# Kernel tuning notes

Hardware: AMD Instinct MI355X
Metric: run time of the kernel (lower is better)

The kernel has to match this reference:

```python
import jax, jax.numpy as jnp
import numpy as np
import math

L, V, P, D, H, B, S = 6, 32000, 1024, 768, 12, 8, 1024
HD = D // H
NEG = jnp.float32(-1e9)
EPS = 1e-5


def gelu(x):
    return 0.5 * x * (1 + jnp.tanh(math.sqrt(2 / math.pi) * (x + 0.044715 * x ** 3)))


def layer_norm(x, g, b):
    mu = jnp.mean(x, -1, keepdims=True)
    var = jnp.mean((x - mu) ** 2, -1, keepdims=True)
    return (x - mu) * jax.lax.rsqrt(var + EPS) * g + b


def setup_inputs() -> dict:
    key = jax.random.key(0)
    ks = jax.random.split(key, 16)
    tokens = jax.random.randint(ks[0], (B, S), 0, V)
    tok_emb = 0.02 * jax.random.normal(ks[1], (V, D), jnp.float32)
    tok_emb = tok_emb.at[0].set(0.0)  # padding_idx=0 row zeroed
    pos_emb = 0.01 * jax.random.normal(ks[2], (P + 1, D), jnp.float32)
    pos_emb = pos_emb.at[0].set(0.0)  # pos padding row
    return {
        "tokens": tokens,
        "tok_emb": tok_emb,
        "pos_emb": pos_emb,
        "qkv_w": 0.02 * jax.random.normal(ks[3], (L, 3 * D, D), jnp.float32),
        "qkv_b": jnp.zeros((L, 3 * D), jnp.float32),
        "out_w": 0.02 * jax.random.normal(ks[4], (L, D, D), jnp.float32),
        "out_b": jnp.zeros((L, D), jnp.float32),
        "ln1_g": jnp.ones((L, D), jnp.float32),
        "ln1_b": jnp.zeros((L, D), jnp.float32),
        "ff1_w": 0.02 * jax.random.normal(ks[5], (L, 4 * D, D), jnp.float32),
        "ff1_b": jnp.zeros((L, 4 * D), jnp.float32),
        "ff2_w": 0.02 * jax.random.normal(ks[6], (L, D, 4 * D), jnp.float32),
        "ff2_b": jnp.zeros((L, D), jnp.float32),
        "ln2_g": jnp.ones((L, D), jnp.float32),
        "ln2_b": jnp.zeros((L, D), jnp.float32),
    }


def _forward(tokens, tok_emb, pos_emb, qkv_w, qkv_b, out_w, out_b,
             ln1_g, ln1_b, ff1_w, ff1_b, ff2_w, ff2_b, ln2_g, ln2_b):
    pad = tokens == 0  # [B,S] padding mask
    positions = jnp.where(pad, 0, jnp.cumsum((~pad).astype(jnp.int32), axis=-1))
    x = tok_emb[tokens] + pos_emb[positions]  # [B,S,D]

    causal = jnp.triu(jnp.ones((S, S), bool), 1)  # future mask
    mask = causal[None, None] | pad[:, None, None, :]  # [B,1,S,S]
    all_masked = mask.all(-1)  # [B,1,S] rows fully -inf -> zeroed after softmax

    def block(x, p):
        qw, qb, ow, ob, g1, b1, f1w, f1b, f2w, f2b, g2, b2 = p
        qkv = x @ qw.T + qb
        q, k, v = jnp.split(qkv, 3, axis=-1)
        q = q.reshape(B, S, H, HD).transpose(0, 2, 1, 3)
        k = k.reshape(B, S, H, HD).transpose(0, 2, 1, 3)
        v = v.reshape(B, S, H, HD).transpose(0, 2, 1, 3)
        w = jnp.einsum('bhqd,bhkd->bhqk', q, k) / math.sqrt(HD)
        w = jnp.where(mask, NEG, w)
        w = jax.nn.softmax(w, axis=-1)
        w = jnp.where(all_masked[..., None], 0.0, w)
        a = jnp.einsum('bhqk,bhkd->bhqd', w, v)
        a = a.transpose(0, 2, 1, 3).reshape(B, S, D)
        a = a @ ow.T + ob
        x = layer_norm(x + a, g1, b1)
        h = gelu(x @ f1w.T + f1b) @ f2w.T + f2b
        x = layer_norm(x + h, g2, b2)
        return x, None

    params = (qkv_w, qkv_b, out_w, out_b, ln1_g, ln1_b,
              ff1_w, ff1_b, ff2_w, ff2_b, ln2_g, ln2_b)
    x, _ = jax.lax.scan(block, x, params)
    return x, pad


def reference(tokens, tok_emb, pos_emb, qkv_w, qkv_b, out_w, out_b,
              ln1_g, ln1_b, ff1_w, ff1_b, ff2_w, ff2_b, ln2_g, ln2_b):
    return _forward(tokens, tok_emb, pos_emb, qkv_w, qkv_b, out_w, out_b,
                    ln1_g, ln1_b, ff1_w, ff1_b, ff2_w, ff2_b, ln2_g, ln2_b)
```

## Files before the change

### kernel.cpp

```cpp
#include <hip/hip_runtime.h>
#include <hip/hip_bf16.h>
#include <math.h>

#define LNUM 6
#define DIM  768
#define HID  3072
#define QKVD 2304
#define NH   12
#define HD   64
#define BB   8
#define SS   1024
#define MTOT (BB*SS)

typedef _Float16 f16x8 __attribute__((ext_vector_type(8)));
typedef _Float16 f16x4 __attribute__((ext_vector_type(4)));
typedef float    f32x4 __attribute__((ext_vector_type(4)));

__device__ __forceinline__ void gload_lds16(const void* g, void* l) {
    __builtin_amdgcn_global_load_lds(
        (const __attribute__((address_space(1))) void*)g,
        (__attribute__((address_space(3))) void*)l, 16, 0, 0);
}

__global__ __launch_bounds__(1024) void pos_kernel(const int* __restrict__ tokens,
                                                   int* __restrict__ positions,
                                                   float* __restrict__ pad_out) {
    const int b = blockIdx.x;
    const int s = threadIdx.x;
    const int tok = tokens[b*SS + s];
    const int np = (tok != 0) ? 1 : 0;
    __shared__ int sc[SS];
    sc[s] = np;
    __syncthreads();
    for (int off = 1; off < SS; off <<= 1) {
        int v = sc[s];
        if (s >= off) v += sc[s - off];
        __syncthreads();
        sc[s] = v;
        __syncthreads();
    }
    positions[b*SS + s] = np ? sc[s] : 0;
    pad_out[b*SS + s]   = np ? 0.0f : 1.0f;
}

__global__ __launch_bounds__(256) void embed_kernel(const int* __restrict__ tokens,
                                                    const int* __restrict__ positions,
                                                    const float* __restrict__ tok_emb,
                                                    const float* __restrict__ pos_emb,
                                                    float* __restrict__ x32,
                                                    _Float16* __restrict__ x16) {
    const int gid = blockIdx.x * 256 + threadIdx.x;
    const int m = gid / (DIM/4);
    const int c = (gid % (DIM/4)) * 4;
    const int tok = tokens[m];
    const int p   = positions[m];
    const float4 te = *(const float4*)(tok_emb + (size_t)tok*DIM + c);
    const float4 pe = *(const float4*)(pos_emb + (size_t)p  *DIM + c);
    float4 r;
    r.x = te.x + pe.x; r.y = te.y + pe.y; r.z = te.z + pe.z; r.w = te.w + pe.w;
    *(float4*)(x32 + (size_t)m*DIM + c) = r;
    f16x4 h; h[0] = (_Float16)r.x; h[1] = (_Float16)r.y; h[2] = (_Float16)r.z; h[3] = (_Float16)r.w;
    *(f16x4*)(x16 + (size_t)m*DIM + c) = h;
}

__global__ __launch_bounds__(256) void cvt16_kernel(const float* __restrict__ in,
                                                    _Float16* __restrict__ out, int n4) {
    const int i = blockIdx.x * 256 + threadIdx.x;
    if (i < n4) {
        const float4 v = ((const float4*)in)[i];
        f16x4 h; h[0] = (_Float16)v.x; h[1] = (_Float16)v.y; h[2] = (_Float16)v.z; h[3] = (_Float16)v.w;
        ((f16x4*)out)[i] = h;
    }
}

template<int EPI>
__global__ __launch_bounds__(256) void hgemm_kernel(const _Float16* __restrict__ A,
                                                    const _Float16* __restrict__ W,
                                                    const float* __restrict__ bias,
                                                    const float* __restrict__ res,
                                                    void* __restrict__ Cout,
                                                    int M, int N, int K) {
    __shared__ char lds[32768];
    const int tid  = threadIdx.x;
    const int w    = tid >> 6;
    const int lane = tid & 63;
    const int wr = w >> 1, wc = w & 1;
    const int bm = blockIdx.y, bn = blockIdx.x;
    const _Float16* Arow = A + (size_t)(bm*128)*K;
    const _Float16* Brow = W + (size_t)(bn*128)*K;

    f32x4 acc[4][4] = {};

    for (int k0 = 0; k0 < K; k0 += 64) {
        #pragma unroll
        for (int i = 0; i < 4; i++) {
            const int p  = (i*4 + w)*64 + lane;
            const int r  = p >> 3;
            const int ul = (p & 7) ^ (r & 7);
            gload_lds16(Arow + (size_t)r*K + k0 + ul*8, lds + (i*4 + w)*1024);
            gload_lds16(Brow + (size_t)r*K + k0 + ul*8, lds + 16384 + (i*4 + w)*1024);
        }
        __syncthreads();
        #pragma unroll
        for (int ks = 0; ks < 2; ks++) {
            f16x8 af[4], bf[4];
            #pragma unroll
            for (int mi = 0; mi < 4; mi++) {
                const int ra = wr*64 + mi*16 + (lane & 15);
                const int ua = (ks*4 + (lane >> 4)) ^ (ra & 7);
                af[mi] = *(const f16x8*)(lds + ra*128 + ua*16);
                const int rb = wc*64 + mi*16 + (lane & 15);
                const int ub = (ks*4 + (lane >> 4)) ^ (rb & 7);
                bf[mi] = *(const f16x8*)(lds + 16384 + rb*128 + ub*16);
            }
            #pragma unroll
            for (int mi = 0; mi < 4; mi++)
                #pragma unroll
                for (int ni = 0; ni < 4; ni++)
                    acc[mi][ni] = __builtin_amdgcn_mfma_f32_16x16x32_f16(af[mi], bf[ni], acc[mi][ni], 0, 0, 0);
        }
        __syncthreads();
    }

    const int lr = lane >> 4, lc = lane & 15;
    #pragma unroll
    for (int mi = 0; mi < 4; mi++) {
        #pragma unroll
        for (int r = 0; r < 4; r++) {
            const int row = bm*128 + wr*64 + mi*16 + lr*4 + r;
            #pragma unroll
            for (int ni = 0; ni < 4; ni++) {
                const int col = bn*128 + wc*64 + ni*16 + lc;
                float v = acc[mi][ni][r] + bias[col];
                if (EPI == 1) v += res[(size_t)row*N + col];
                if (EPI == 2) {
                    const float u = v;
                    v = 0.5f*u*(1.0f + tanhf(0.7978845608028654f*(u + 0.044715f*u*u*u)));
                    ((_Float16*)Cout)[(size_t)row*N + col] = (_Float16)v;
                } else {
                    ((float*)Cout)[(size_t)row*N + col] = v;
                }
            }
        }
    }
}

__global__ __launch_bounds__(256) void attn_kernel(const float* __restrict__ qkv,
                                                   const int* __restrict__ tokens,
                                                   _Float16* __restrict__ aout) {
    __shared__ float Ks[64][64];
    __shared__ float Vs[64][64];
    __shared__ int tf[64];
    const int gx = blockIdx.x;
    const int qblk = 3 - (gx / 96);
    const int bh = gx % 96;
    const int h = bh % NH, b = bh / NH;
    const int w = threadIdx.x >> 6, lane = threadIdx.x & 63;
    const int ql = qblk*256 + lane*4 + w;
    const size_t rowq = (size_t)(b*SS + ql);
    const float* kv0 = qkv + (size_t)b*SS*QKVD + DIM + h*HD;

    f32x4 qv[16];
    const float* qp = qkv + rowq*QKVD + h*HD;
    #pragma unroll
    for (int i = 0; i < 16; i++) {
        qv[i] = *(const f32x4*)(qp + i*4);
        qv[i] *= 0.125f;
    }
    f32x4 av[16] = {};
    float m = -1e30f, lsum = 0.0f;

    const int ntile = qblk*4 + 4;
    for (int t = 0; t < ntile; t++) {
        const int k0 = t*64;
        __syncthreads();
        for (int p4 = threadIdx.x; p4 < 1024; p4 += 256) {
            const int r = p4 >> 4, c = (p4 & 15)*4;
            const float* src = kv0 + (size_t)(k0 + r)*QKVD + c;
            *(float4*)&Ks[r][c] = *(const float4*)src;
            *(float4*)&Vs[r][c] = *(const float4*)(src + DIM);
        }
        if (threadIdx.x < 64) tf[threadIdx.x] = tokens[b*SS + k0 + threadIdx.x];
        __syncthreads();
        for (int kk = 0; kk < 64; kk++) {
            if (tf[kk] == 0) continue;
            const int k = k0 + kk;
            f32x4 s4 = {};
            #pragma unroll
            for (int i = 0; i < 16; i++)
                s4 += qv[i] * *(const f32x4*)&Ks[kk][i*4];
            const float s = (s4[0] + s4[1]) + (s4[2] + s4[3]);
            const bool valid = (k <= ql);
            if (valid && s > m + 8.0f) {
                const float f = __expf(m - s);
                lsum *= f;
                #pragma unroll
                for (int i = 0; i < 16; i++) av[i] *= f;
                m = s;
            }
            const float p = valid ? __expf(s - m) : 0.0f;
            lsum += p;
            #pragma unroll
            for (int i = 0; i < 16; i++)
                av[i] += p * *(const f32x4*)&Vs[kk][i*4];
        }
    }
    const float inv = (lsum > 0.0f) ? 1.0f / lsum : 0.0f;
    _Float16* op = aout + rowq*DIM + h*HD;
    #pragma unroll
    for (int i = 0; i < 16; i++) {
        f16x4 o;
        o[0] = (_Float16)(av[i][0]*inv); o[1] = (_Float16)(av[i][1]*inv);
        o[2] = (_Float16)(av[i][2]*inv); o[3] = (_Float16)(av[i][3]*inv);
        *(f16x4*)(op + i*4) = o;
    }
}

__global__ __launch_bounds__(256) void ln_kernel(const float* __restrict__ in,
                                                 const float* __restrict__ g,
                                                 const float* __restrict__ b,
                                                 float* __restrict__ out32,
                                                 _Float16* __restrict__ out16) {
    const int row = blockIdx.x;
    const int t = threadIdx.x;
    const float* xr = in + (size_t)row*DIM;
    const float v0 = xr[t], v1 = xr[t+256], v2 = xr[t+512];
    __shared__ float red[4];
    __shared__ float stat[2];
    const int lane = t & 63, wid = t >> 6;
    float s = v0 + v1 + v2;
    #pragma unroll
    for (int off = 32; off; off >>= 1) s += __shfl_down(s, off);
    if (lane == 0) red[wid] = s;
    __syncthreads();
    if (t == 0) stat[0] = (red[0]+red[1]+red[2]+red[3]) * (1.0f/DIM);
    __syncthreads();
    const float mean = stat[0];
    const float d0 = v0-mean, d1 = v1-mean, d2 = v2-mean;
    float sq = d0*d0 + d1*d1 + d2*d2;
    #pragma unroll
    for (int off = 32; off; off >>= 1) sq += __shfl_down(sq, off);
    __syncthreads();
    if (lane == 0) red[wid] = sq;
    __syncthreads();
    if (t == 0) stat[1] = rsqrtf((red[0]+red[1]+red[2]+red[3]) * (1.0f/DIM) + 1e-5f);
    __syncthreads();
    const float rstd = stat[1];
    float* orow = out32 + (size_t)row*DIM;
    _Float16* hrow = out16 + (size_t)row*DIM;
    const float o0 = d0*rstd*g[t]     + b[t];
    const float o1 = d1*rstd*g[t+256] + b[t+256];
    const float o2 = d2*rstd*g[t+512] + b[t+512];
    orow[t]     = o0; orow[t+256] = o1; orow[t+512] = o2;
    hrow[t]     = (_Float16)o0; hrow[t+256] = (_Float16)o1; hrow[t+512] = (_Float16)o2;
}

extern "C" void kernel_launch(void* const* d_in, const int* in_sizes, int n_in,
                              void* d_out, int out_size, void* d_ws, size_t ws_size,
                              hipStream_t stream) {
    const int*   tokens  = (const int*)  d_in[0];
    const float* tok_emb = (const float*)d_in[1];
    const float* pos_emb = (const float*)d_in[2];
    const float* qkv_w   = (const float*)d_in[3];
    const float* qkv_b   = (const float*)d_in[4];
    const float* out_w   = (const float*)d_in[5];
    const float* out_b   = (const float*)d_in[6];
    const float* ln1_g   = (const float*)d_in[7];
    const float* ln1_b   = (const float*)d_in[8];
    const float* ff1_w   = (const float*)d_in[9];
    const float* ff1_b   = (const float*)d_in[10];
    const float* ff2_w   = (const float*)d_in[11];
    const float* ff2_b   = (const float*)d_in[12];
    const float* ln2_g   = (const float*)d_in[13];
    const float* ln2_b   = (const float*)d_in[14];

    char* ws = (char*)d_ws;
    size_t off = 0;
    auto carve = [&](size_t bytes) { char* p = ws + off; off += (bytes + 255) & ~(size_t)255; return p; };
    int*      positions = (int*)     carve((size_t)MTOT*4);
    float*    x32    = (float*)      carve((size_t)MTOT*DIM*4);
    _Float16* x16    = (_Float16*)   carve((size_t)MTOT*DIM*2);
    float*    ln1o32 = (float*)      carve((size_t)MTOT*DIM*4);
    _Float16* ln1o16 = (_Float16*)   carve((size_t)MTOT*DIM*2);
    float*    y32    = (float*)      carve((size_t)MTOT*DIM*4);
    float*    qkv32  = (float*)      carve((size_t)MTOT*QKVD*4);
    _Float16* a16    = (_Float16*)   carve((size_t)MTOT*DIM*2);
    _Float16* h16    = (_Float16*)   carve((size_t)MTOT*HID*2);
    _Float16* wq16   = (_Float16*)   carve((size_t)QKVD*DIM*2);
    _Float16* wo16   = (_Float16*)   carve((size_t)DIM*DIM*2);
    _Float16* w116   = (_Float16*)   carve((size_t)HID*DIM*2);
    _Float16* w216   = (_Float16*)   carve((size_t)DIM*HID*2);

    float* outx    = (float*)d_out;
    float* pad_out = outx + (size_t)MTOT*DIM;

    pos_kernel<<<BB, SS, 0, stream>>>(tokens, positions, pad_out);
    embed_kernel<<<(MTOT*(DIM/4))/256, 256, 0, stream>>>(tokens, positions, tok_emb, pos_emb, x32, x16);

    for (int l = 0; l < LNUM; l++) {
        cvt16_kernel<<<(QKVD*DIM/4)/256, 256, 0, stream>>>(qkv_w + (size_t)l*QKVD*DIM, wq16, QKVD*DIM/4);
        cvt16_kernel<<<(DIM*DIM/4)/256,  256, 0, stream>>>(out_w + (size_t)l*DIM*DIM,  wo16, DIM*DIM/4);
        cvt16_kernel<<<(HID*DIM/4)/256,  256, 0, stream>>>(ff1_w + (size_t)l*HID*DIM,  w116, HID*DIM/4);
        cvt16_kernel<<<(DIM*HID/4)/256,  256, 0, stream>>>(ff2_w + (size_t)l*DIM*HID,  w216, DIM*HID/4);

        hgemm_kernel<0><<<dim3(QKVD/128, MTOT/128), 256, 0, stream>>>(
            x16, wq16, qkv_b + (size_t)l*QKVD, nullptr, qkv32, MTOT, QKVD, DIM);
        attn_kernel<<<BB*NH*4, 256, 0, stream>>>(qkv32, tokens, a16);
        hgemm_kernel<1><<<dim3(DIM/128, MTOT/128), 256, 0, stream>>>(
            a16, wo16, out_b + (size_t)l*DIM, x32, y32, MTOT, DIM, DIM);
        ln_kernel<<<MTOT, 256, 0, stream>>>(y32, ln1_g + (size_t)l*DIM, ln1_b + (size_t)l*DIM, ln1o32, ln1o16);
        hgemm_kernel<2><<<dim3(HID/128, MTOT/128), 256, 0, stream>>>(
            ln1o16, w116, ff1_b + (size_t)l*HID, nullptr, h16, MTOT, HID, DIM);
        hgemm_kernel<1><<<dim3(DIM/128, MTOT/128), 256, 0, stream>>>(
            h16, w216, ff2_b + (size_t)l*DIM, ln1o32, y32, MTOT, DIM, HID);
        ln_kernel<<<MTOT, 256, 0, stream>>>(
            y32, ln2_g + (size_t)l*DIM, ln2_b + (size_t)l*DIM, (l == LNUM-1) ? outx : x32, x16);
    }
}
```

Before: 5.309 ms.

## Split attention into split-K partial kernel with combine pass and fp16 keys

The QKV GEMM now writes Q and V as separate fp32 buffers and K as fp16. Attention is restructured from one thread per query over 256-query blocks into 64-query tiles whose key range is split across four waves, each keeping its own running softmax state. A second kernel merges the four partials. Keys are read straight from global memory and scored with fp16 dot2 instructions, with no LDS staging or block barriers. This raises parallelism and balances causal work, at the cost of extra partial-result traffic through a scratch buffer aliased with h16, fp16 rounding of Q and K scores, and uncoalesced per-thread row loads.

```diff
diff --git a/kernel.cpp b/kernel.cpp
--- a/kernel.cpp
+++ b/kernel.cpp
@@ -14,7 +14,18 @@
 
 typedef _Float16 f16x8 __attribute__((ext_vector_type(8)));
 typedef _Float16 f16x4 __attribute__((ext_vector_type(4)));
+typedef _Float16 h2    __attribute__((ext_vector_type(2)));
 typedef float    f32x4 __attribute__((ext_vector_type(4)));
+
+struct h2x4 { h2 x[4]; };
+
+__device__ __forceinline__ float fdot2f(h2 a, h2 b, float c) {
+#if __has_builtin(__builtin_amdgcn_fdot2)
+    return __builtin_amdgcn_fdot2(a, b, c, false);
+#else
+    return c + (float)a[0]*(float)b[0] + (float)a[1]*(float)b[1];
+#endif
+}
 
 __device__ __forceinline__ void gload_lds16(const void* g, void* l) {
     __builtin_amdgcn_global_load_lds(
@@ -79,6 +90,8 @@
                                                     const float* __restrict__ bias,
                                                     const float* __restrict__ res,
                                                     void* __restrict__ Cout,
+                                                    void* __restrict__ CoutB,
+                                                    void* __restrict__ CoutC,
                                                     int M, int N, int K) {
     __shared__ char lds[32768];
     const int tid  = threadIdx.x;
@@ -137,6 +150,10 @@
                     const float u = v;
                     v = 0.5f*u*(1.0f + tanhf(0.7978845608028654f*(u + 0.044715f*u*u*u)));
                     ((_Float16*)Cout)[(size_t)row*N + col] = (_Float16)v;
+                } else if (EPI == 3) {
+                    if (col < DIM)            ((float*)Cout)[(size_t)row*DIM + col] = v;
+                    else if (col < 2*DIM) ((_Float16*)CoutB)[(size_t)row*DIM + col - DIM] = (_Float16)v;
+                    else                     ((float*)CoutC)[(size_t)row*DIM + col - 2*DIM] = v;
                 } else {
                     ((float*)Cout)[(size_t)row*N + col] = v;
                 }
@@ -145,73 +162,134 @@
     }
 }
 
-__global__ __launch_bounds__(256) void attn_kernel(const float* __restrict__ qkv,
-                                                   const int* __restrict__ tokens,
-                                                   _Float16* __restrict__ aout) {
-    __shared__ float Ks[64][64];
-    __shared__ float Vs[64][64];
-    __shared__ int tf[64];
-    const int gx = blockIdx.x;
-    const int qblk = 3 - (gx / 96);
-    const int bh = gx % 96;
+__global__ __launch_bounds__(256, 3) void attn_part_kernel(const float* __restrict__ q32,
+                                                           const _Float16* __restrict__ k16,
+                                                           const float* __restrict__ v32,
+                                                           const int* __restrict__ tokens,
+                                                           float* __restrict__ part_av,
+                                                           float* __restrict__ part_ml) {
+    const int bx = blockIdx.x;
+    const int qt = 15 - (bx & 15);
+    const int bh = bx >> 4;
     const int h = bh % NH, b = bh / NH;
-    const int w = threadIdx.x >> 6, lane = threadIdx.x & 63;
-    const int ql = qblk*256 + lane*4 + w;
+    const int tid = threadIdx.x;
+    const int w = __builtin_amdgcn_readfirstlane(tid >> 6);
+    const int lane = tid & 63;
+    const int ql = qt*64 + lane;
     const size_t rowq = (size_t)(b*SS + ql);
-    const float* kv0 = qkv + (size_t)b*SS*QKVD + DIM + h*HD;
-
-    f32x4 qv[16];
-    const float* qp = qkv + rowq*QKVD + h*HD;
-    #pragma unroll
-    for (int i = 0; i < 16; i++) {
-        qv[i] = *(const f32x4*)(qp + i*4);
-        qv[i] *= 0.125f;
-    }
+
+    const float* qp = q32 + rowq*DIM + h*HD;
+    h2 qh[32];
+    #pragma unroll
+    for (int i = 0; i < 32; i++) {
+        qh[i][0] = (_Float16)(qp[2*i]   * 0.125f);
+        qh[i][1] = (_Float16)(qp[2*i+1] * 0.125f);
+    }
+
     f32x4 av[16] = {};
     float m = -1e30f, lsum = 0.0f;
 
-    const int ntile = qblk*4 + 4;
-    for (int t = 0; t < ntile; t++) {
+    const int ntiles = qt + 1;
+    const int per = (ntiles + 3) >> 2;
+    const int t0 = w * per;
+    const int t1 = (t0 + per < ntiles) ? t0 + per : ntiles;
+
+    const _Float16* kb = k16 + (size_t)(b*SS)*DIM + h*HD;
+    const float*    vb = v32 + (size_t)(b*SS)*DIM + h*HD;
+    const int*     tkp = tokens + b*SS;
+
+    for (int t = t0; t < t1; t++) {
         const int k0 = t*64;
-        __syncthreads();
-        for (int p4 = threadIdx.x; p4 < 1024; p4 += 256) {
-            const int r = p4 >> 4, c = (p4 & 15)*4;
-            const float* src = kv0 + (size_t)(k0 + r)*QKVD + c;
-            *(float4*)&Ks[r][c] = *(const float4*)src;
-            *(float4*)&Vs[r][c] = *(const float4*)(src + DIM);
+        #pragma unroll 1
+        for (int g = 0; g < 16; g++) {
+            const int4 t4 = *(const int4*)(tkp + k0 + g*4);
+            #pragma unroll
+            for (int c = 0; c < 4; c++) {
+                const int k = k0 + g*4 + c;
+                const int tok = (c==0) ? t4.x : (c==1) ? t4.y : (c==2) ? t4.z : t4.w;
+                const f16x8* kr8 = (const f16x8*)(kb + (size_t)k*DIM);
+                float s0 = 0.f, s1 = 0.f, s2 = 0.f, s3 = 0.f;
+                #pragma unroll
+                for (int j = 0; j < 8; j++) {
+                    const h2x4 kc = __builtin_bit_cast(h2x4, kr8[j]);
+                    s0 = fdot2f(qh[j*4+0], kc.x[0], s0);
+                    s1 = fdot2f(qh[j*4+1], kc.x[1], s1);
+                    s2 = fdot2f(qh[j*4+2], kc.x[2], s2);
+                    s3 = fdot2f(qh[j*4+3], kc.x[3], s3);
+                }
+                const float s = (s0 + s1) + (s2 + s3);
+                const bool valid = (tok != 0) && (k <= ql);
+                if (valid && s > m + 8.0f) {
+                    const float f = __expf(m - s);
+                    lsum *= f;
+                    #pragma unroll
+                    for (int i = 0; i < 16; i++) av[i] *= f;
+                    m = s;
+                }
+                const float p = valid ? __expf(s - m) : 0.0f;
+                lsum += p;
+                const float* vr = vb + (size_t)k*DIM;
+                #pragma unroll
+                for (int i = 0; i < 16; i++)
+                    av[i] += p * *(const f32x4*)(vr + i*4);
+            }
         }
-        if (threadIdx.x < 64) tf[threadIdx.x] = tokens[b*SS + k0 + threadIdx.x];
-        __syncthreads();
-        for (int kk = 0; kk < 64; kk++) {
-            if (tf[kk] == 0) continue;
-            const int k = k0 + kk;
-            f32x4 s4 = {};
-            #pragma unroll
-            for (int i = 0; i < 16; i++)
-                s4 += qv[i] * *(const f32x4*)&Ks[kk][i*4];
-            const float s = (s4[0] + s4[1]) + (s4[2] + s4[3]);
-            const bool valid = (k <= ql);
-            if (valid && s > m + 8.0f) {
-                const float f = __expf(m - s);
-                lsum *= f;
-                #pragma unroll
-                for (int i = 0; i < 16; i++) av[i] *= f;
-                m = s;
-            }
-            const float p = valid ? __expf(s - m) : 0.0f;
-            lsum += p;
-            #pragma unroll
-            for (int i = 0; i < 16; i++)
-                av[i] += p * *(const f32x4*)&Vs[kk][i*4];
+    }
+
+    const size_t job = (size_t)bx*4 + w;
+    float* pav = part_av + job*4096;
+    #pragma unroll
+    for (int i = 0; i < 16; i++)
+        #pragma unroll
+        for (int c = 0; c < 4; c++)
+            pav[(i*4 + c)*64 + lane] = av[i][c];
+    part_ml[job*128 + lane*2]     = m;
+    part_ml[job*128 + lane*2 + 1] = lsum;
+}
+
+__global__ __launch_bounds__(256) void attn_comb_kernel(const float* __restrict__ part_av,
+                                                        const float* __restrict__ part_ml,
+                                                        _Float16* __restrict__ aout) {
+    const int jobIdx = blockIdx.x*4 + (threadIdx.x >> 6);
+    const int lane = threadIdx.x & 63;
+    const int qt = 15 - (jobIdx & 15);
+    const int bh = jobIdx >> 4;
+    const int h = bh % NH, b = bh / NH;
+    const int ql = qt*64 + lane;
+
+    float ms[4], ls[4];
+    #pragma unroll
+    for (int s = 0; s < 4; s++) {
+        const size_t j = (size_t)jobIdx*4 + s;
+        ms[s] = part_ml[j*128 + lane*2];
+        ls[s] = part_ml[j*128 + lane*2 + 1];
+    }
+    const float M = fmaxf(fmaxf(ms[0], ms[1]), fmaxf(ms[2], ms[3]));
+    float ws[4];
+    #pragma unroll
+    for (int s = 0; s < 4; s++) ws[s] = __expf(ms[s] - M);
+    const float L = ls[0]*ws[0] + ls[1]*ws[1] + ls[2]*ws[2] + ls[3]*ws[3];
+    const float inv = (L > 0.0f) ? 1.0f / L : 0.0f;
+    #pragma unroll
+    for (int s = 0; s < 4; s++) ws[s] *= inv;
+
+    _Float16* op = aout + (size_t)(b*SS + ql)*DIM + h*HD;
+    #pragma unroll
+    for (int i = 0; i < 16; i++) {
+        f32x4 acc = {};
+        #pragma unroll
+        for (int s = 0; s < 4; s++) {
+            const float* pav = part_av + ((size_t)jobIdx*4 + s)*4096;
+            f32x4 v;
+            v[0] = pav[(i*4+0)*64 + lane];
+            v[1] = pav[(i*4+1)*64 + lane];
+            v[2] = pav[(i*4+2)*64 + lane];
+            v[3] = pav[(i*4+3)*64 + lane];
+            acc += ws[s] * v;
         }
-    }
-    const float inv = (lsum > 0.0f) ? 1.0f / lsum : 0.0f;
-    _Float16* op = aout + rowq*DIM + h*HD;
-    #pragma unroll
-    for (int i = 0; i < 16; i++) {
         f16x4 o;
-        o[0] = (_Float16)(av[i][0]*inv); o[1] = (_Float16)(av[i][1]*inv);
-        o[2] = (_Float16)(av[i][2]*inv); o[3] = (_Float16)(av[i][3]*inv);
+        o[0] = (_Float16)acc[0]; o[1] = (_Float16)acc[1];
+        o[2] = (_Float16)acc[2]; o[3] = (_Float16)acc[3];
         *(f16x4*)(op + i*4) = o;
     }
 }
@@ -283,9 +361,14 @@
     float*    ln1o32 = (float*)      carve((size_t)MTOT*DIM*4);
     _Float16* ln1o16 = (_Float16*)   carve((size_t)MTOT*DIM*2);
     float*    y32    = (float*)      carve((size_t)MTOT*DIM*4);
-    float*    qkv32  = (float*)      carve((size_t)MTOT*QKVD*4);
+    float*    q32    = (float*)      carve((size_t)MTOT*DIM*4);
+    _Float16* k16    = (_Float16*)   carve((size_t)MTOT*DIM*2);
+    float*    v32    = (float*)      carve((size_t)MTOT*DIM*4);
     _Float16* a16    = (_Float16*)   carve((size_t)MTOT*DIM*2);
-    _Float16* h16    = (_Float16*)   carve((size_t)MTOT*HID*2);
+    char*     R      =               carve((size_t)6144*4096*4 + (size_t)6144*128*4);
+    float*    part_av = (float*)R;
+    float*    part_ml = (float*)(R + (size_t)6144*4096*4);
+    _Float16* h16     = (_Float16*)R;
     _Float16* wq16   = (_Float16*)   carve((size_t)QKVD*DIM*2);
     _Float16* wo16   = (_Float16*)   carve((size_t)DIM*DIM*2);
     _Float16* w116   = (_Float16*)   carve((size_t)HID*DIM*2);
@@ -303,16 +386,17 @@
         cvt16_kernel<<<(HID*DIM/4)/256,  256, 0, stream>>>(ff1_w + (size_t)l*HID*DIM,  w116, HID*DIM/4);
         cvt16_kernel<<<(DIM*HID/4)/256,  256, 0, stream>>>(ff2_w + (size_t)l*DIM*HID,  w216, DIM*HID/4);
 
-        hgemm_kernel<0><<<dim3(QKVD/128, MTOT/128), 256, 0, stream>>>(
-            x16, wq16, qkv_b + (size_t)l*QKVD, nullptr, qkv32, MTOT, QKVD, DIM);
-        attn_kernel<<<BB*NH*4, 256, 0, stream>>>(qkv32, tokens, a16);
+        hgemm_kernel<3><<<dim3(QKVD/128, MTOT/128), 256, 0, stream>>>(
+            x16, wq16, qkv_b + (size_t)l*QKVD, nullptr, q32, k16, v32, MTOT, QKVD, DIM);
+        attn_part_kernel<<<BB*NH*16, 256, 0, stream>>>(q32, k16, v32, tokens, part_av, part_ml);
+        attn_comb_kernel<<<BB*NH*4, 256, 0, stream>>>(part_av, part_ml, a16);
         hgemm_kernel<1><<<dim3(DIM/128, MTOT/128), 256, 0, stream>>>(
-            a16, wo16, out_b + (size_t)l*DIM, x32, y32, MTOT, DIM, DIM);
+            a16, wo16, out_b + (size_t)l*DIM, x32, y32, nullptr, nullptr, MTOT, DIM, DIM);
         ln_kernel<<<MTOT, 256, 0, stream>>>(y32, ln1_g + (size_t)l*DIM, ln1_b + (size_t)l*DIM, ln1o32, ln1o16);
         hgemm_kernel<2><<<dim3(HID/128, MTOT/128), 256, 0, stream>>>(
-            ln1o16, w116, ff1_b + (size_t)l*HID, nullptr, h16, MTOT, HID, DIM);
+            ln1o16, w116, ff1_b + (size_t)l*HID, nullptr, h16, nullptr, nullptr, MTOT, HID, DIM);
         hgemm_kernel<1><<<dim3(DIM/128, MTOT/128), 256, 0, stream>>>(
-            h16, w216, ff2_b + (size_t)l*DIM, ln1o32, y32, MTOT, DIM, HID);
+            h16, w216, ff2_b + (size_t)l*DIM, ln1o32, y32, nullptr, nullptr, MTOT, DIM, HID);
         ln_kernel<<<MTOT, 256, 0, stream>>>(
             y32, ln2_g + (size_t)l*DIM, ln2_b + (size_t)l*DIM, (l == LNUM-1) ? outx : x32, x16);
     }
```

Result: slower. 6.694 ms (+26.1%).
